# Performance work log

Measured on AMD Instinct MI355X. Metric: run time of the kernel, lower is better.

The kernel has to match this reference:

```python
import jax, jax.numpy as jnp
import numpy as np

N, E, D, H, ED = 50000, 800000, 128, 16, 16
TAU = 0.5

def _seg_sum(data, ids, n):
    return jax.ops.segment_sum(data, ids, num_segments=n)

def gcn_conv(x, src, dst, ew, W, b, n):
    # PyG-style GCNConv with added self-loops (weight 1) and symmetric normalization
    xw = x @ W                                   # [n, out]
    deg = _seg_sum(ew, dst, n) + 1.0             # in-degree incl. self-loop
    dinv = jax.lax.rsqrt(deg)
    norm = dinv[src] * ew * dinv[dst]            # [E]
    out = _seg_sum(xw[src] * norm[:, None], dst, n)
    out = out + xw * (dinv * dinv)[:, None]      # self-loop message
    return out + b

def layer_norm(x, g, b, eps=1e-5):
    mu = jnp.mean(x, -1, keepdims=True)
    var = jnp.mean((x - mu) ** 2, -1, keepdims=True)
    return (x - mu) * jax.lax.rsqrt(var + eps) * g + b

def gumbel_hard(logits, u, tau):
    # F.gumbel_softmax(hard=True) with straight-through estimator
    g = -jnp.log(-jnp.log(u + 1e-10) + 1e-10)
    y = jax.nn.softmax((logits + g) / tau, axis=-1)
    hard = jax.nn.one_hot(jnp.argmax(y, -1), y.shape[-1], dtype=y.dtype)
    return hard + y - jax.lax.stop_gradient(y)

def action_net(x, src, dst, w1, b1, w2, b2, n):
    ones = jnp.ones((src.shape[0],), x.dtype)
    h = jax.nn.relu(gcn_conv(x, src, dst, ones, w1, b1, n))
    return gcn_conv(h, src, dst, ones, w2, b2, n)    # [n, 2]

def setup_inputs():
    key = jax.random.key(0)
    ks = jax.random.split(key, 12)
    p = lambda k, s: (0.02 * jax.random.normal(k, s)).astype(jnp.float32)
    return dict(
        x=jax.random.normal(ks[0], (N, D), jnp.float32),
        edge_index=jax.random.randint(ks[1], (2, E), 0, N, jnp.int32),
        edge_attr=jax.random.normal(ks[2], (E, ED), jnp.float32),
        u_in=jax.random.uniform(ks[3], (N, 2), jnp.float32),
        u_out=jax.random.uniform(ks[4], (N, 2), jnp.float32),
        ln_g=jnp.ones((D,), jnp.float32), ln_b=jnp.zeros((D,), jnp.float32),
        conv_w=p(ks[5], (D, D)), conv_b=jnp.zeros((D,), jnp.float32),
        ep_w=p(ks[6], (ED, D)), ep_b=jnp.zeros((D,), jnp.float32),
        ia1_w=p(ks[7], (D, H)), ia1_b=jnp.zeros((H,), jnp.float32),
        ia2_w=p(ks[8], (H, 2)), ia2_b=jnp.zeros((2,), jnp.float32),
        oa1_w=p(ks[9], (D, H)), oa1_b=jnp.zeros((H,), jnp.float32),
        oa2_w=p(ks[10], (H, 2)), oa2_b=jnp.zeros((2,), jnp.float32),
    )

def reference(x, edge_index, edge_attr, u_in, u_out, ln_g, ln_b, conv_w, conv_b,
              ep_w, ep_b, ia1_w, ia1_b, ia2_w, ia2_b, oa1_w, oa1_b, oa2_w, oa2_b):
    src, dst = edge_index[0], edge_index[1]
    # edge_proj (dropout is identity in eval mode)
    edge_features = jax.nn.relu(edge_attr @ ep_w + ep_b)      # [E, D]
    xn = layer_norm(x, ln_g, ln_b)
    in_logits = action_net(xn, src, dst, ia1_w, ia1_b, ia2_w, ia2_b, N)
    out_logits = action_net(xn, src, dst, oa1_w, oa1_b, oa2_w, oa2_b, N)
    in_probs = gumbel_hard(in_logits, u_in, TAU)
    out_probs = gumbel_hard(out_logits, u_out, TAU)
    edge_weight = in_probs[dst, 0] * out_probs[src, 0]        # [E]
    out = gcn_conv(xn, src, dst, edge_weight, conv_w, conv_b, N)
    out = out + _seg_sum(edge_features, dst, N)
    return jax.nn.relu(out)
```

## Files before the change

### kernel.cpp

```cpp
#include <hip/hip_runtime.h>
#include <hip/hip_bf16.h>

#define DD 128
#define HH 16
#define SCAN_B 1024
#define TPW 8

typedef __bf16 bf16x8 __attribute__((ext_vector_type(8)));
typedef float f32x4 __attribute__((ext_vector_type(4)));

__global__ void ln_kernel(const float* __restrict__ x, const float* __restrict__ g,
                          const float* __restrict__ b, float* __restrict__ xn, int n_nodes) {
  int w = (blockIdx.x * blockDim.x + threadIdx.x) >> 6;
  int lane = threadIdx.x & 63;
  if (w >= n_nodes) return;
  const float* xr = x + (size_t)w * DD;
  float a0 = xr[lane], a1 = xr[lane + 64];
  float s = a0 + a1;
  #pragma unroll
  for (int o = 32; o > 0; o >>= 1) s += __shfl_down(s, o);
  s = __shfl(s, 0);
  float mu = s * (1.0f / DD);
  float d0 = a0 - mu, d1 = a1 - mu;
  float v = d0 * d0 + d1 * d1;
  #pragma unroll
  for (int o = 32; o > 0; o >>= 1) v += __shfl_down(v, o);
  v = __shfl(v, 0);
  float rstd = rsqrtf(v * (1.0f / DD) + 1e-5f);
  float* xo = xn + (size_t)w * DD;
  xo[lane]      = d0 * rstd * g[lane] + b[lane];
  xo[lane + 64] = d1 * rstd * g[lane + 64] + b[lane + 64];
}

__global__ __launch_bounds__(256) void proj1_kernel(const float* __restrict__ xn,
    const float* __restrict__ ia1_w, const float* __restrict__ oa1_w,
    float* __restrict__ xw_a, int n_nodes) {
  __shared__ __align__(16) float wl[DD * 32];
  for (int i = threadIdx.x; i < DD * HH; i += 256) {
    int dd = i >> 4, jj = i & 15;
    wl[dd * 32 + jj]      = ia1_w[i];
    wl[dd * 32 + 16 + jj] = oa1_w[i];
  }
  __syncthreads();
  int t = blockIdx.x * blockDim.x + threadIdx.x;
  int n = t >> 5, j = t & 31;
  if (n >= n_nodes) return;
  const float* xr = xn + (size_t)n * DD;
  float acc = 0.f;
  #pragma unroll 8
  for (int d = 0; d < DD; ++d) acc = fmaf(xr[d], wl[d * 32 + j], acc);
  xw_a[(size_t)n * 32 + j] = acc;
}

__global__ void degcnt_kernel(const int* __restrict__ dst, int* __restrict__ deg, int n_edges) {
  int e = blockIdx.x * blockDim.x + threadIdx.x;
  if (e < n_edges) atomicAdd(&deg[dst[e]], 1);
}

__global__ __launch_bounds__(SCAN_B) void scan1_kernel(const int* __restrict__ deg,
    int* __restrict__ rs, int* __restrict__ partials, int n_nodes) {
  __shared__ int sm[SCAN_B];
  int i = blockIdx.x * SCAN_B + threadIdx.x;
  int v = (i < n_nodes) ? deg[i] : 0;
  sm[threadIdx.x] = v;
  __syncthreads();
  for (int o = 1; o < SCAN_B; o <<= 1) {
    int t = (threadIdx.x >= o) ? sm[threadIdx.x - o] : 0;
    __syncthreads();
    sm[threadIdx.x] += t;
    __syncthreads();
  }
  if (i < n_nodes) rs[i] = sm[threadIdx.x] - v;
  if (threadIdx.x == SCAN_B - 1) partials[blockIdx.x] = sm[threadIdx.x];
}

__global__ __launch_bounds__(SCAN_B) void scan2_kernel(int* __restrict__ partials, int nb) {
  __shared__ int sm[SCAN_B];
  int v = (threadIdx.x < nb) ? partials[threadIdx.x] : 0;
  sm[threadIdx.x] = v;
  __syncthreads();
  for (int o = 1; o < SCAN_B; o <<= 1) {
    int t = (threadIdx.x >= o) ? sm[threadIdx.x - o] : 0;
    __syncthreads();
    sm[threadIdx.x] += t;
    __syncthreads();
  }
  if (threadIdx.x < nb) partials[threadIdx.x] = sm[threadIdx.x] - v;
}

__global__ __launch_bounds__(SCAN_B) void scan3_kernel(int* __restrict__ rs,
    const int* __restrict__ partials, int n_nodes) {
  int i = blockIdx.x * SCAN_B + threadIdx.x;
  if (i < n_nodes) rs[i] += partials[blockIdx.x];
}

__global__ void fill_kernel(const int* __restrict__ src, const int* __restrict__ dst,
    int* __restrict__ rs, int* __restrict__ csr_eid, int* __restrict__ csr_src, int n_edges) {
  int e = blockIdx.x * blockDim.x + threadIdx.x;
  if (e >= n_edges) return;
  int d = dst[e];
  int pos = atomicAdd(&rs[d], 1);
  csr_eid[pos] = e;
  csr_src[pos] = src[e];
}

__global__ void dinva_kernel(const int* __restrict__ deg, float* __restrict__ dinv, int n_nodes) {
  int i = blockIdx.x * blockDim.x + threadIdx.x;
  if (i < n_nodes) dinv[i] = rsqrtf((float)deg[i] + 1.0f);
}

__global__ __launch_bounds__(256) void agg1_kernel(const int* __restrict__ rs,
    const int* __restrict__ deg, const int* __restrict__ csr_src,
    const float* __restrict__ xw_a, const float* __restrict__ dinva,
    const float* __restrict__ ia1_b, const float* __restrict__ oa1_b,
    const float* __restrict__ ia2_w, const float* __restrict__ oa2_w,
    float* __restrict__ xw2_a, int n_nodes) {
  int t = blockIdx.x * blockDim.x + threadIdx.x;
  int node = t >> 5, j = t & 31;
  if (node >= n_nodes) return;
  int dg = deg[node];
  int st = rs[node] - dg;
  float acc = 0.f;
  for (int i = 0; i < dg; ++i) {
    int s = csr_src[st + i];
    acc = fmaf(xw_a[(size_t)s * 32 + j], dinva[s], acc);
  }
  float di = dinva[node];
  float bias = (j < 16) ? ia1_b[j] : oa1_b[j - 16];
  float h = fmaxf(acc * di + xw_a[(size_t)node * 32 + j] * di * di + bias, 0.f);
  float w0 = (j < 16) ? ia2_w[j * 2 + 0] : oa2_w[(j - 16) * 2 + 0];
  float w1 = (j < 16) ? ia2_w[j * 2 + 1] : oa2_w[(j - 16) * 2 + 1];
  float p0 = h * w0, p1 = h * w1;
  #pragma unroll
  for (int o = 1; o < 16; o <<= 1) { p0 += __shfl_xor(p0, o); p1 += __shfl_xor(p1, o); }
  if ((j & 15) == 0) {
    int k = j >> 4;
    xw2_a[(size_t)node * 4 + k * 2 + 0] = p0;
    xw2_a[(size_t)node * 4 + k * 2 + 1] = p1;
  }
}

__global__ void agg2_kernel(const int* __restrict__ rs, const int* __restrict__ deg,
    const int* __restrict__ csr_src, const float* __restrict__ xw2_a,
    const float* __restrict__ dinva, const float* __restrict__ ia2_b,
    const float* __restrict__ oa2_b, const float* __restrict__ u_in,
    const float* __restrict__ u_out, float* __restrict__ fin, float* __restrict__ fout,
    int n_nodes) {
  int t = blockIdx.x * blockDim.x + threadIdx.x;
  int node = t >> 4, l = t & 15;
  if (node >= n_nodes) return;
  int dg = deg[node];
  int st = rs[node] - dg;
  float a0 = 0.f, a1 = 0.f, a2 = 0.f, a3 = 0.f;
  for (int i = l; i < dg; i += 16) {
    int s = csr_src[st + i];
    float ds = dinva[s];
    float4 v = *(const float4*)&xw2_a[(size_t)s * 4];
    a0 = fmaf(v.x, ds, a0); a1 = fmaf(v.y, ds, a1);
    a2 = fmaf(v.z, ds, a2); a3 = fmaf(v.w, ds, a3);
  }
  #pragma unroll
  for (int o = 1; o < 16; o <<= 1) {
    a0 += __shfl_xor(a0, o); a1 += __shfl_xor(a1, o);
    a2 += __shfl_xor(a2, o); a3 += __shfl_xor(a3, o);
  }
  if (l == 0) {
    float di = dinva[node], sw = di * di;
    float4 self = *(const float4*)&xw2_a[(size_t)node * 4];
    float li0 = a0 * di + self.x * sw + ia2_b[0];
    float li1 = a1 * di + self.y * sw + ia2_b[1];
    float lo0 = a2 * di + self.z * sw + oa2_b[0];
    float lo1 = a3 * di + self.w * sw + oa2_b[1];
    float gi0 = -logf(-logf(u_in[(size_t)node * 2 + 0] + 1e-10f) + 1e-10f);
    float gi1 = -logf(-logf(u_in[(size_t)node * 2 + 1] + 1e-10f) + 1e-10f);
    float go0 = -logf(-logf(u_out[(size_t)node * 2 + 0] + 1e-10f) + 1e-10f);
    float go1 = -logf(-logf(u_out[(size_t)node * 2 + 1] + 1e-10f) + 1e-10f);
    fin[node]  = (li0 + gi0 >= li1 + gi1) ? 1.f : 0.f;
    fout[node] = (lo0 + go0 >= lo1 + go1) ? 1.f : 0.f;
  }
}

__global__ void cdeg_kernel(const int* __restrict__ rs, const int* __restrict__ deg,
    const int* __restrict__ csr_src, const float* __restrict__ fin,
    const float* __restrict__ fout, float* __restrict__ dinvc, int n_nodes) {
  int t = blockIdx.x * blockDim.x + threadIdx.x;
  int node = t >> 4, l = t & 15;
  if (node >= n_nodes) return;
  int dg = deg[node];
  int st = rs[node] - dg;
  float c = 0.f;
  if (fin[node] != 0.f) {
    for (int i = l; i < dg; i += 16) c += (fout[csr_src[st + i]] != 0.f) ? 1.f : 0.f;
  }
  #pragma unroll
  for (int o = 1; o < 16; o <<= 1) c += __shfl_xor(c, o);
  if (l == 0) dinvc[node] = rsqrtf(c + 1.0f);
}

#define GEMM_ROWS 64
__global__ __launch_bounds__(256) void gemm_kernel(const float* __restrict__ xn,
    const float* __restrict__ W, float* __restrict__ xwc, int n_nodes) {
  __shared__ __align__(16) float wl[DD * DD];
  for (int i = threadIdx.x * 4; i < DD * DD; i += 256 * 4)
    *(float4*)&wl[i] = *(const float4*)&W[i];
  __syncthreads();
  int c4 = (threadIdx.x & 31) * 4;
  int r0 = threadIdx.x >> 5;
  int base = blockIdx.x * GEMM_ROWS;
  for (int r = r0; r < GEMM_ROWS; r += 8) {
    int n = base + r;
    if (n >= n_nodes) break;
    const float* xr = xn + (size_t)n * DD;
    float4 acc = {0.f, 0.f, 0.f, 0.f};
    #pragma unroll 4
    for (int d = 0; d < DD; ++d) {
      float xv = xr[d];
      float4 w = *(const float4*)&wl[d * DD + c4];
      acc.x = fmaf(xv, w.x, acc.x);
      acc.y = fmaf(xv, w.y, acc.y);
      acc.z = fmaf(xv, w.z, acc.z);
      acc.w = fmaf(xv, w.w, acc.w);
    }
    *(float4*)&xwc[(size_t)n * DD + c4] = acc;
  }
}

__global__ __launch_bounds__(256) void mlp_kernel(const int* __restrict__ csr_eid,
    const float* __restrict__ ea, const float* __restrict__ ep_w,
    const float* __restrict__ ep_b, __bf16* __restrict__ ef, int n_edges) {
  int l = threadIdx.x & 63;
  int wave_g = (blockIdx.x * 256 + threadIdx.x) >> 6;
  int tile0 = wave_g * TPW;
  int col = l & 15;
  int kg = l >> 4;
  int k0 = kg * 8;
  bool a_active = (k0 < HH);
  bf16x8 bfr[8];
  float bias[8];
  #pragma unroll
  for (int nt = 0; nt < 8; ++nt) {
    int j = nt * 16 + col;
    bf16x8 bb;
    #pragma unroll
    for (int i = 0; i < 8; ++i) {
      int k = k0 + i;
      bb[i] = (__bf16)((k < HH) ? ep_w[k * DD + j] : 0.f);
    }
    bfr[nt] = bb;
    bias[nt] = ep_b[j];
  }
  for (int t = 0; t < TPW; ++t) {
    int pos0 = (tile0 + t) * 16;
    if (pos0 >= n_edges) return;
    int apos = pos0 + col;
    int eid = csr_eid[(apos < n_edges) ? apos : (n_edges - 1)];
    bf16x8 afr = {};
    if (a_active) {
      const float4* er = (const float4*)(ea + (size_t)eid * HH + k0);
      float4 f0 = er[0], f1 = er[1];
      afr[0] = (__bf16)f0.x; afr[1] = (__bf16)f0.y;
      afr[2] = (__bf16)f0.z; afr[3] = (__bf16)f0.w;
      afr[4] = (__bf16)f1.x; afr[5] = (__bf16)f1.y;
      afr[6] = (__bf16)f1.z; afr[7] = (__bf16)f1.w;
    }
    #pragma unroll
    for (int nt = 0; nt < 8; ++nt) {
      f32x4 d = {0.f, 0.f, 0.f, 0.f};
      d = __builtin_amdgcn_mfma_f32_16x16x32_bf16(afr, bfr[nt], d, 0, 0, 0);
      int j = nt * 16 + col;
      #pragma unroll
      for (int r = 0; r < 4; ++r) {
        int pos = pos0 + kg * 4 + r;
        if (pos < n_edges)
          ef[(size_t)pos * DD + j] = (__bf16)fmaxf(d[r] + bias[nt], 0.f);
      }
    }
  }
}

__global__ __launch_bounds__(256) void kbig_kernel(const int* __restrict__ rs,
    const int* __restrict__ deg, const int* __restrict__ csr_src,
    const __bf16* __restrict__ ef, const float* __restrict__ xwc,
    const float* __restrict__ dinvc, const float* __restrict__ fin,
    const float* __restrict__ fout, const float* __restrict__ conv_b,
    float* __restrict__ out, int n_nodes) {
  int node = (blockIdx.x * blockDim.x + threadIdx.x) >> 6;
  int l = threadIdx.x & 63;
  if (node >= n_nodes) return;
  int dg = deg[node];
  int st = rs[node] - dg;
  float fd = fin[node];
  float dj = dinvc[node];
  float a0 = 0.f, a1 = 0.f, c0 = 0.f, c1 = 0.f;
  for (int i = 0; i < dg; ++i) {
    int pos = st + i;
    unsigned u = *(const unsigned*)(ef + (size_t)pos * DD + 2 * l);
    a0 += __uint_as_float(u << 16);
    a1 += __uint_as_float(u & 0xffff0000u);
    if (fd != 0.f) {
      int s = csr_src[pos];
      if (fout[s] != 0.f) {
        float2 w = *(const float2*)(xwc + (size_t)s * DD + 2 * l);
        float ds = dinvc[s];
        c0 = fmaf(w.x, ds, c0);
        c1 = fmaf(w.y, ds, c1);
      }
    }
  }
  float2 selfw = *(const float2*)(xwc + (size_t)node * DD + 2 * l);
  float2 cb = *(const float2*)(conv_b + 2 * l);
  float o0 = a0 + c0 * dj + selfw.x * dj * dj + cb.x;
  float o1 = a1 + c1 * dj + selfw.y * dj * dj + cb.y;
  float2 res = {fmaxf(o0, 0.f), fmaxf(o1, 0.f)};
  *(float2*)(out + (size_t)node * DD + 2 * l) = res;
}

__global__ __launch_bounds__(256) void kbig_fused_kernel(const int* __restrict__ rs,
    const int* __restrict__ deg, const int* __restrict__ csr_src,
    const int* __restrict__ csr_eid, const float* __restrict__ ea,
    const float* __restrict__ ep_w, const float* __restrict__ ep_b,
    const float* __restrict__ xwc, const float* __restrict__ dinvc,
    const float* __restrict__ fin, const float* __restrict__ fout,
    const float* __restrict__ conv_b, float* __restrict__ out, int n_nodes) {
  __shared__ __align__(16) float wl[HH * DD];
  __shared__ float bl[DD];
  for (int i = threadIdx.x; i < HH * DD; i += 256) wl[i] = ep_w[i];
  if (threadIdx.x < DD) bl[threadIdx.x] = ep_b[threadIdx.x];
  __syncthreads();
  int t = blockIdx.x * blockDim.x + threadIdx.x;
  int node = t >> 7, j = t & 127;
  if (node >= n_nodes) return;
  int dg = deg[node];
  int st = rs[node] - dg;
  float fd = fin[node];
  float dj = dinvc[node];
  float aed = 0.f, acv = 0.f;
  for (int i = 0; i < dg; ++i) {
    int e = csr_eid[st + i];
    int s = csr_src[st + i];
    const float4* ear = (const float4*)(ea + (size_t)e * HH);
    float4 e0 = ear[0], e1 = ear[1], e2 = ear[2], e3 = ear[3];
    float m = bl[j];
    m = fmaf(e0.x, wl[0 * DD + j], m); m = fmaf(e0.y, wl[1 * DD + j], m);
    m = fmaf(e0.z, wl[2 * DD + j], m); m = fmaf(e0.w, wl[3 * DD + j], m);
    m = fmaf(e1.x, wl[4 * DD + j], m); m = fmaf(e1.y, wl[5 * DD + j], m);
    m = fmaf(e1.z, wl[6 * DD + j], m); m = fmaf(e1.w, wl[7 * DD + j], m);
    m = fmaf(e2.x, wl[8 * DD + j], m); m = fmaf(e2.y, wl[9 * DD + j], m);
    m = fmaf(e2.z, wl[10 * DD + j], m); m = fmaf(e2.w, wl[11 * DD + j], m);
    m = fmaf(e3.x, wl[12 * DD + j], m); m = fmaf(e3.y, wl[13 * DD + j], m);
    m = fmaf(e3.z, wl[14 * DD + j], m); m = fmaf(e3.w, wl[15 * DD + j], m);
    aed += fmaxf(m, 0.f);
    if (fd != 0.f) {
      if (fout[s] != 0.f) acv = fmaf(xwc[(size_t)s * DD + j], dinvc[s], acv);
    }
  }
  float v = aed + acv * dj + xwc[(size_t)node * DD + j] * dj * dj + conv_b[j];
  out[(size_t)node * DD + j] = fmaxf(v, 0.f);
}

extern "C" void kernel_launch(void* const* d_in, const int* in_sizes, int n_in,
                              void* d_out, int out_size, void* d_ws, size_t ws_size,
                              hipStream_t stream) {
  const float* x      = (const float*)d_in[0];
  const int*   eidx   = (const int*)d_in[1];
  const float* ea     = (const float*)d_in[2];
  const float* u_in   = (const float*)d_in[3];
  const float* u_out  = (const float*)d_in[4];
  const float* ln_g   = (const float*)d_in[5];
  const float* ln_b   = (const float*)d_in[6];
  const float* conv_w = (const float*)d_in[7];
  const float* conv_b = (const float*)d_in[8];
  const float* ep_w   = (const float*)d_in[9];
  const float* ep_b   = (const float*)d_in[10];
  const float* ia1_w  = (const float*)d_in[11];
  const float* ia1_b  = (const float*)d_in[12];
  const float* ia2_w  = (const float*)d_in[13];
  const float* ia2_b  = (const float*)d_in[14];
  const float* oa1_w  = (const float*)d_in[15];
  const float* oa1_b  = (const float*)d_in[16];
  const float* oa2_w  = (const float*)d_in[17];
  const float* oa2_b  = (const float*)d_in[18];

  const int n = in_sizes[0] / DD;
  const int E = in_sizes[1] / 2;
  const int* src = eidx;
  const int* dst = eidx + E;

  float* ws = (float*)d_ws;
  float* xn    = ws;
  float* xw_a  = xn + (size_t)n * 128;
  float* xw2_a = xw_a + (size_t)n * 32;
  float* dinva = xw2_a + (size_t)n * 4;
  float* xwc   = dinva + n;
  int* deg_i   = (int*)(xwc + (size_t)n * 128);
  int* rs      = deg_i + n;
  int* partials= rs + n;
  int* csr_eid = partials + 1024;
  int* csr_src = csr_eid + E;
  __bf16* ef   = (__bf16*)(csr_src + E);
  float* fin   = xw_a;
  float* fout  = xw_a + n;
  float* dinvc = xw_a + 2 * (size_t)n;

  float* out = (float*)d_out;

  size_t need = ((size_t)n * 295 + 2 * (size_t)E + 1024) * 4 + (size_t)E * DD * 2;
  bool big_ws = ws_size >= need;

  hipMemsetAsync(deg_i, 0, (size_t)n * sizeof(int), stream);

  const int B = 256;
  const int nb = (n + SCAN_B - 1) / SCAN_B;

  ln_kernel<<<(n * 64 + B - 1) / B, B, 0, stream>>>(x, ln_g, ln_b, xn, n);
  proj1_kernel<<<(n * 32 + B - 1) / B, B, 0, stream>>>(xn, ia1_w, oa1_w, xw_a, n);
  degcnt_kernel<<<(E + B - 1) / B, B, 0, stream>>>(dst, deg_i, E);
  scan1_kernel<<<nb, SCAN_B, 0, stream>>>(deg_i, rs, partials, n);
  scan2_kernel<<<1, SCAN_B, 0, stream>>>(partials, nb);
  scan3_kernel<<<nb, SCAN_B, 0, stream>>>(rs, partials, n);
  dinva_kernel<<<(n + B - 1) / B, B, 0, stream>>>(deg_i, dinva, n);
  fill_kernel<<<(E + B - 1) / B, B, 0, stream>>>(src, dst, rs, csr_eid, csr_src, E);
  agg1_kernel<<<(n * 32 + B - 1) / B, B, 0, stream>>>(rs, deg_i, csr_src, xw_a, dinva,
                                                      ia1_b, oa1_b, ia2_w, oa2_w, xw2_a, n);
  agg2_kernel<<<(n * 16 + B - 1) / B, B, 0, stream>>>(rs, deg_i, csr_src, xw2_a, dinva,
                                                      ia2_b, oa2_b, u_in, u_out, fin, fout, n);
  cdeg_kernel<<<(n * 16 + B - 1) / B, B, 0, stream>>>(rs, deg_i, csr_src, fin, fout, dinvc, n);
  gemm_kernel<<<(n + GEMM_ROWS - 1) / GEMM_ROWS, B, 0, stream>>>(xn, conv_w, xwc, n);

  if (big_ws) {
    int tiles = (E + 15) / 16;
    int nwaves = (tiles + TPW - 1) / TPW;
    int nblocks = (nwaves + 3) / 4;
    mlp_kernel<<<nblocks, B, 0, stream>>>(csr_eid, ea, ep_w, ep_b, ef, E);
    kbig_kernel<<<((size_t)n * 64 + B - 1) / B, B, 0, stream>>>(rs, deg_i, csr_src, ef,
        xwc, dinvc, fin, fout, conv_b, out, n);
  } else {
    kbig_fused_kernel<<<((size_t)n * DD + B - 1) / B, B, 0, stream>>>(rs, deg_i, csr_src,
        csr_eid, ea, ep_w, ep_b, xwc, dinvc, fin, fout, conv_b, out, n);
  }
}
```

Measured before the change: 773.6 us.

## Fuse edge MLP with CSR aggregation via edge-partitioned blocks and LDS staging

Replaces the separate edge-MLP kernel, which wrote a bf16 [E,128] buffer to global memory, and the node-gather kernel with one edge-partitioned kernel. Each block computes 256 edges' MFMA projections into LDS, then walks the CSR segments covering those edges, summing edge features and the gated conv messages. It writes a node's row directly when the block holds the whole segment and uses atomicAdd when a segment spans blocks. A final elementwise kernel adds the self-loop term and bias and applies ReLU. This removes the large global round-trip for edge features at the cost of an extra output memset, a per-block binary search, per-segment barriers and some atomics.

```diff
diff --git a/kernel.cpp b/kernel.cpp
--- a/kernel.cpp
+++ b/kernel.cpp
@@ -4,7 +4,8 @@
 #define DD 128
 #define HH 16
 #define SCAN_B 1024
-#define TPW 8
+#define EPB 256
+#define VT_STRIDE 132
 
 typedef __bf16 bf16x8 __attribute__((ext_vector_type(8)));
 typedef float f32x4 __attribute__((ext_vector_type(4)));
@@ -225,137 +226,121 @@
   }
 }
 
-__global__ __launch_bounds__(256) void mlp_kernel(const int* __restrict__ csr_eid,
+__global__ __launch_bounds__(256) void edgenode_kernel(
+    const int* __restrict__ rs, const int* __restrict__ deg,
+    const int* __restrict__ csr_src, const int* __restrict__ csr_eid,
     const float* __restrict__ ea, const float* __restrict__ ep_w,
-    const float* __restrict__ ep_b, __bf16* __restrict__ ef, int n_edges) {
-  int l = threadIdx.x & 63;
-  int wave_g = (blockIdx.x * 256 + threadIdx.x) >> 6;
-  int tile0 = wave_g * TPW;
-  int col = l & 15;
-  int kg = l >> 4;
-  int k0 = kg * 8;
-  bool a_active = (k0 < HH);
-  bf16x8 bfr[8];
-  float bias[8];
-  #pragma unroll
-  for (int nt = 0; nt < 8; ++nt) {
-    int j = nt * 16 + col;
-    bf16x8 bb;
+    const float* __restrict__ ep_b, const float* __restrict__ xwc,
+    const float* __restrict__ dinvc, const float* __restrict__ fin,
+    const float* __restrict__ fout, float* __restrict__ out_acc,
+    int n_nodes, int n_edges) {
+  __shared__ __align__(16) __bf16 vt[EPB * VT_STRIDE];
+  __shared__ float comb[2][DD];
+  const int tid = threadIdx.x;
+  const int P = blockIdx.x * EPB;
+  const int Pend = min(P + EPB, n_edges);
+
+  {
+    const int l = tid & 63;
+    const int w = tid >> 6;
+    const int col = l & 15;
+    const int kg = l >> 4;
+    const int k0 = kg * 8;
+    bf16x8 bfr[8];
+    float bias[8];
     #pragma unroll
-    for (int i = 0; i < 8; ++i) {
-      int k = k0 + i;
-      bb[i] = (__bf16)((k < HH) ? ep_w[k * DD + j] : 0.f);
-    }
-    bfr[nt] = bb;
-    bias[nt] = ep_b[j];
-  }
-  for (int t = 0; t < TPW; ++t) {
-    int pos0 = (tile0 + t) * 16;
-    if (pos0 >= n_edges) return;
-    int apos = pos0 + col;
-    int eid = csr_eid[(apos < n_edges) ? apos : (n_edges - 1)];
-    bf16x8 afr = {};
-    if (a_active) {
-      const float4* er = (const float4*)(ea + (size_t)eid * HH + k0);
-      float4 f0 = er[0], f1 = er[1];
-      afr[0] = (__bf16)f0.x; afr[1] = (__bf16)f0.y;
-      afr[2] = (__bf16)f0.z; afr[3] = (__bf16)f0.w;
-      afr[4] = (__bf16)f1.x; afr[5] = (__bf16)f1.y;
-      afr[6] = (__bf16)f1.z; afr[7] = (__bf16)f1.w;
+    for (int nt = 0; nt < 8; ++nt) {
+      int j = nt * 16 + col;
+      bf16x8 bb = {};
+      if (k0 < HH) {
+        #pragma unroll
+        for (int i = 0; i < 8; ++i) bb[i] = (__bf16)ep_w[(k0 + i) * DD + j];
+      }
+      bfr[nt] = bb;
+      bias[nt] = ep_b[j];
     }
     #pragma unroll
-    for (int nt = 0; nt < 8; ++nt) {
-      f32x4 d = {0.f, 0.f, 0.f, 0.f};
-      d = __builtin_amdgcn_mfma_f32_16x16x32_bf16(afr, bfr[nt], d, 0, 0, 0);
-      int j = nt * 16 + col;
-      #pragma unroll
-      for (int r = 0; r < 4; ++r) {
-        int pos = pos0 + kg * 4 + r;
-        if (pos < n_edges)
-          ef[(size_t)pos * DD + j] = (__bf16)fmaxf(d[r] + bias[nt], 0.f);
+    for (int t = 0; t < 4; ++t) {
+      int tile = w * 4 + t;
+      int pos0 = P + tile * 16;
+      if (pos0 < n_edges) {
+        int apos = pos0 + col;
+        int eid = csr_eid[(apos < n_edges) ? apos : (n_edges - 1)];
+        bf16x8 afr = {};
+        if (k0 < HH) {
+          const float4* er = (const float4*)(ea + (size_t)eid * HH + k0);
+          float4 f0 = er[0], f1 = er[1];
+          afr[0] = (__bf16)f0.x; afr[1] = (__bf16)f0.y;
+          afr[2] = (__bf16)f0.z; afr[3] = (__bf16)f0.w;
+          afr[4] = (__bf16)f1.x; afr[5] = (__bf16)f1.y;
+          afr[6] = (__bf16)f1.z; afr[7] = (__bf16)f1.w;
+        }
+        #pragma unroll
+        for (int nt = 0; nt < 8; ++nt) {
+          f32x4 d4 = {0.f, 0.f, 0.f, 0.f};
+          d4 = __builtin_amdgcn_mfma_f32_16x16x32_bf16(afr, bfr[nt], d4, 0, 0, 0);
+          #pragma unroll
+          for (int r = 0; r < 4; ++r) {
+            int rowl = tile * 16 + kg * 4 + r;
+            vt[rowl * VT_STRIDE + nt * 16 + col] = (__bf16)fmaxf(d4[r] + bias[nt], 0.f);
+          }
+        }
       }
     }
   }
-}
-
-__global__ __launch_bounds__(256) void kbig_kernel(const int* __restrict__ rs,
-    const int* __restrict__ deg, const int* __restrict__ csr_src,
-    const __bf16* __restrict__ ef, const float* __restrict__ xwc,
-    const float* __restrict__ dinvc, const float* __restrict__ fin,
-    const float* __restrict__ fout, const float* __restrict__ conv_b,
-    float* __restrict__ out, int n_nodes) {
-  int node = (blockIdx.x * blockDim.x + threadIdx.x) >> 6;
-  int l = threadIdx.x & 63;
-  if (node >= n_nodes) return;
-  int dg = deg[node];
-  int st = rs[node] - dg;
-  float fd = fin[node];
-  float dj = dinvc[node];
-  float a0 = 0.f, a1 = 0.f, c0 = 0.f, c1 = 0.f;
-  for (int i = 0; i < dg; ++i) {
-    int pos = st + i;
-    unsigned u = *(const unsigned*)(ef + (size_t)pos * DD + 2 * l);
-    a0 += __uint_as_float(u << 16);
-    a1 += __uint_as_float(u & 0xffff0000u);
+  __syncthreads();
+
+  const int j = tid & 127;
+  const int h = tid >> 7;
+  int lo = 0, hi = n_nodes;
+  while (lo < hi) {
+    int mid = (lo + hi) >> 1;
+    if (rs[mid] > P) hi = mid; else lo = mid + 1;
+  }
+  int d = lo;
+  int p = P;
+  int seg = 0;
+  while (p < Pend) {
+    int re = rs[d];
+    if (re <= p) { ++d; continue; }
+    int se = (re < Pend) ? re : Pend;
+    float fd = fin[d] * dinvc[d];
+    float sum = 0.f;
+    int pstart = p + (((p & 1) == h) ? 0 : 1);
     if (fd != 0.f) {
-      int s = csr_src[pos];
-      if (fout[s] != 0.f) {
-        float2 w = *(const float2*)(xwc + (size_t)s * DD + 2 * l);
-        float ds = dinvc[s];
-        c0 = fmaf(w.x, ds, c0);
-        c1 = fmaf(w.y, ds, c1);
+      for (int p2 = pstart; p2 < se; p2 += 2) {
+        sum += (float)vt[(p2 - P) * VT_STRIDE + j];
+        int s = csr_src[p2];
+        float fs = fout[s];
+        if (fs != 0.f) sum = fmaf(fd * dinvc[s], xwc[(size_t)s * DD + j], sum);
       }
+    } else {
+      for (int p2 = pstart; p2 < se; p2 += 2)
+        sum += (float)vt[(p2 - P) * VT_STRIDE + j];
     }
-  }
-  float2 selfw = *(const float2*)(xwc + (size_t)node * DD + 2 * l);
-  float2 cb = *(const float2*)(conv_b + 2 * l);
-  float o0 = a0 + c0 * dj + selfw.x * dj * dj + cb.x;
-  float o1 = a1 + c1 * dj + selfw.y * dj * dj + cb.y;
-  float2 res = {fmaxf(o0, 0.f), fmaxf(o1, 0.f)};
-  *(float2*)(out + (size_t)node * DD + 2 * l) = res;
-}
-
-__global__ __launch_bounds__(256) void kbig_fused_kernel(const int* __restrict__ rs,
-    const int* __restrict__ deg, const int* __restrict__ csr_src,
-    const int* __restrict__ csr_eid, const float* __restrict__ ea,
-    const float* __restrict__ ep_w, const float* __restrict__ ep_b,
-    const float* __restrict__ xwc, const float* __restrict__ dinvc,
-    const float* __restrict__ fin, const float* __restrict__ fout,
-    const float* __restrict__ conv_b, float* __restrict__ out, int n_nodes) {
-  __shared__ __align__(16) float wl[HH * DD];
-  __shared__ float bl[DD];
-  for (int i = threadIdx.x; i < HH * DD; i += 256) wl[i] = ep_w[i];
-  if (threadIdx.x < DD) bl[threadIdx.x] = ep_b[threadIdx.x];
-  __syncthreads();
+    int k = seg & 1;
+    if (h == 1) comb[k][j] = sum;
+    __syncthreads();
+    if (h == 0) {
+      float total = sum + comb[k][j];
+      bool full = (se == re) && (p == re - deg[d]);
+      if (full) out_acc[(size_t)d * DD + j] = total;
+      else atomicAdd(&out_acc[(size_t)d * DD + j], total);
+    }
+    p = se;
+    if (se == re) ++d;
+    ++seg;
+  }
+}
+
+__global__ void final_kernel(float* __restrict__ out_acc, const float* __restrict__ xwc,
+    const float* __restrict__ dinvc, const float* __restrict__ conv_b, int n_nodes) {
   int t = blockIdx.x * blockDim.x + threadIdx.x;
-  int node = t >> 7, j = t & 127;
-  if (node >= n_nodes) return;
-  int dg = deg[node];
-  int st = rs[node] - dg;
-  float fd = fin[node];
-  float dj = dinvc[node];
-  float aed = 0.f, acv = 0.f;
-  for (int i = 0; i < dg; ++i) {
-    int e = csr_eid[st + i];
-    int s = csr_src[st + i];
-    const float4* ear = (const float4*)(ea + (size_t)e * HH);
-    float4 e0 = ear[0], e1 = ear[1], e2 = ear[2], e3 = ear[3];
-    float m = bl[j];
-    m = fmaf(e0.x, wl[0 * DD + j], m); m = fmaf(e0.y, wl[1 * DD + j], m);
-    m = fmaf(e0.z, wl[2 * DD + j], m); m = fmaf(e0.w, wl[3 * DD + j], m);
-    m = fmaf(e1.x, wl[4 * DD + j], m); m = fmaf(e1.y, wl[5 * DD + j], m);
-    m = fmaf(e1.z, wl[6 * DD + j], m); m = fmaf(e1.w, wl[7 * DD + j], m);
-    m = fmaf(e2.x, wl[8 * DD + j], m); m = fmaf(e2.y, wl[9 * DD + j], m);
-    m = fmaf(e2.z, wl[10 * DD + j], m); m = fmaf(e2.w, wl[11 * DD + j], m);
-    m = fmaf(e3.x, wl[12 * DD + j], m); m = fmaf(e3.y, wl[13 * DD + j], m);
-    m = fmaf(e3.z, wl[14 * DD + j], m); m = fmaf(e3.w, wl[15 * DD + j], m);
-    aed += fmaxf(m, 0.f);
-    if (fd != 0.f) {
-      if (fout[s] != 0.f) acv = fmaf(xwc[(size_t)s * DD + j], dinvc[s], acv);
-    }
-  }
-  float v = aed + acv * dj + xwc[(size_t)node * DD + j] * dj * dj + conv_b[j];
-  out[(size_t)node * DD + j] = fmaxf(v, 0.f);
+  if (t >= n_nodes * DD) return;
+  int n = t >> 7, j = t & 127;
+  float di = dinvc[n];
+  float v = out_acc[t] + xwc[t] * di * di + conv_b[j];
+  out_acc[t] = fmaxf(v, 0.f);
 }
 
 extern "C" void kernel_launch(void* const* d_in, const int* in_sizes, int n_in,
@@ -397,17 +382,14 @@
   int* partials= rs + n;
   int* csr_eid = partials + 1024;
   int* csr_src = csr_eid + E;
-  __bf16* ef   = (__bf16*)(csr_src + E);
   float* fin   = xw_a;
   float* fout  = xw_a + n;
   float* dinvc = xw_a + 2 * (size_t)n;
 
-  float* out = (float*)d_out;
-
-  size_t need = ((size_t)n * 295 + 2 * (size_t)E + 1024) * 4 + (size_t)E * DD * 2;
-  bool big_ws = ws_size >= need;
+  float* out_acc = (float*)d_out;
 
   hipMemsetAsync(deg_i, 0, (size_t)n * sizeof(int), stream);
+  hipMemsetAsync(d_out, 0, (size_t)out_size * sizeof(float), stream);
 
   const int B = 256;
   const int nb = (n + SCAN_B - 1) / SCAN_B;
@@ -426,16 +408,7 @@
                                                       ia2_b, oa2_b, u_in, u_out, fin, fout, n);
   cdeg_kernel<<<(n * 16 + B - 1) / B, B, 0, stream>>>(rs, deg_i, csr_src, fin, fout, dinvc, n);
   gemm_kernel<<<(n + GEMM_ROWS - 1) / GEMM_ROWS, B, 0, stream>>>(xn, conv_w, xwc, n);
-
-  if (big_ws) {
-    int tiles = (E + 15) / 16;
-    int nwaves = (tiles + TPW - 1) / TPW;
-    int nblocks = (nwaves + 3) / 4;
-    mlp_kernel<<<nblocks, B, 0, stream>>>(csr_eid, ea, ep_w, ep_b, ef, E);
-    kbig_kernel<<<((size_t)n * 64 + B - 1) / B, B, 0, stream>>>(rs, deg_i, csr_src, ef,
-        xwc, dinvc, fin, fout, conv_b, out, n);
-  } else {
-    kbig_fused_kernel<<<((size_t)n * DD + B - 1) / B, B, 0, stream>>>(rs, deg_i, csr_src,
-        csr_eid, ea, ep_w, ep_b, xwc, dinvc, fin, fout, conv_b, out, n);
-  }
-}
+  edgenode_kernel<<<(E + EPB - 1) / EPB, B, 0, stream>>>(rs, deg_i, csr_src, csr_eid,
+      ea, ep_w, ep_b, xwc, dinvc, fin, fout, out_acc, n, E);
+  final_kernel<<<((size_t)n * DD + B - 1) / B, B, 0, stream>>>(out_acc, xwc, dinvc, conv_b, n);
+}
```

New measurement: 786.1 us. No clear change (+1.6%).
